# Optimization experiments

Hardware: AMD Instinct MI355X
Metric: run time of the kernel (lower is better)

Reference implementation:

```python
import jax, jax.numpy as jnp
import numpy as np

# Dimensions (match input_specs / init_kwargs)
B, T, M, H, E, K = 4, 2048, 1024, 2048, 8, 2
CAP_FACTOR = 1.0  # tutel default capacity_factor
S = B * T
C = int(K * CAP_FACTOR * ((S + E - 1) // E))  # per-expert capacity (tutel Top-k gate)


def setup_inputs() -> dict:
    key = jax.random.key(0)
    ks = jax.random.split(key, 4)
    x = jax.random.normal(ks[0], (B, T, M), jnp.float32)
    wg = jax.random.normal(ks[1], (M, E), jnp.float32) / np.sqrt(M)
    w1 = jax.random.normal(ks[2], (E, M, H), jnp.float32) / np.sqrt(M)
    b1 = jnp.zeros((E, H), jnp.float32)
    w2 = jax.random.normal(ks[3], (E, H, M), jnp.float32) / np.sqrt(H)
    b2 = jnp.zeros((E, M), jnp.float32)
    return {"x": x, "wg": wg, "w1": w1, "b1": b1, "w2": w2, "b2": b2}


def reference(x, wg, w1, b1, w2, b2):
    xf = x.reshape(S, M)
    # ---- Top-k gate (fp32 gate) ----
    logits = xf.astype(jnp.float32) @ wg                 # [S, E]
    scores = jax.nn.softmax(logits, axis=-1)
    topv, topi = jax.lax.top_k(scores, K)                # [S, K]
    gates = topv / (jnp.sum(topv, axis=-1, keepdims=True) + 1e-9)  # normalized top-k gates

    # ---- Dispatch into [E, C, M] buffer with capacity-based token dropping ----
    buf = jnp.zeros((E, C, M), xf.dtype)
    offset = jnp.zeros((E,), jnp.int32)  # tokens already placed per expert (previous slots)
    pos_list, keep_list = [], []
    for j in range(K):  # small fixed loop over top-k slots
        e = topi[:, j]                                   # [S]
        m = jax.nn.one_hot(e, E, dtype=jnp.int32)        # [S, E]
        pos = jnp.sum(jnp.cumsum(m, axis=0) * m, axis=1) - 1 + offset[e]  # position within expert
        offset = offset + jnp.sum(m, axis=0)
        keep = pos < C                                   # drop tokens over capacity
        posc = jnp.minimum(pos, C - 1)
        buf = buf.at[e, posc].add(xf * keep[:, None].astype(xf.dtype))
        pos_list.append(posc)
        keep_list.append(keep)

    # ---- Grouped expert FFN: relu(x W1 + b1) W2 + b2 ----
    h = jax.nn.relu(jnp.einsum('ecm,emh->ech', buf, w1) + b1[:, None, :])  # [E, C, H]
    y = jnp.einsum('ech,ehm->ecm', h, w2) + b2[:, None, :]                 # [E, C, M]

    # ---- Combine with gate weights ----
    out = jnp.zeros_like(xf)
    for j in range(K):
        g = gates[:, j] * keep_list[j].astype(xf.dtype)
        out = out + g[:, None] * y[topi[:, j], pos_list[j]]

    out = out.reshape(B, T, M)
    # result = log_softmax(sum over model_dim, over token dim)
    return jax.nn.log_softmax(jnp.sum(out, axis=2), axis=1)   # [B, T]
```

## Files before the change

kernel.cpp:

```cpp
#include <hip/hip_runtime.h>
#include <hip/hip_bf16.h>
#include <cstdint>
#include <cstddef>

constexpr int Bb = 4;
constexpr int Tt = 2048;
constexpr int Mm = 1024;
constexpr int Hh = 2048;
constexpr int Ee = 8;
constexpr int Ss = Bb * Tt;
constexpr int Cc = 2048;

typedef __attribute__((ext_vector_type(4))) float f32x4;
typedef __attribute__((ext_vector_type(8))) short bf16x8;

__device__ inline void load_lds16(const void* g, void* l) {
    __builtin_amdgcn_global_load_lds(
        (const __attribute__((address_space(1))) unsigned int*)g,
        (__attribute__((address_space(3))) unsigned int*)l, 16, 0, 0);
}

__global__ __launch_bounds__(256) void k_w1t(const float* __restrict__ w1,
                                             __hip_bfloat16* __restrict__ w1t) {
    __shared__ float tile[64][65];
    int e = blockIdx.z, m0 = blockIdx.y * 64, h0 = blockIdx.x * 64;
    int t = threadIdx.x;
    const float* src = w1 + (size_t)e * Mm * Hh;
    #pragma unroll
    for (int i = 0; i < 4; i++) {
        int idx = t + i * 256;
        int r = idx >> 4, c4 = idx & 15;
        float4 v = *(const float4*)(src + (size_t)(m0 + r) * Hh + h0 + c4 * 4);
        tile[r][c4 * 4 + 0] = v.x; tile[r][c4 * 4 + 1] = v.y;
        tile[r][c4 * 4 + 2] = v.z; tile[r][c4 * 4 + 3] = v.w;
    }
    __syncthreads();
    __hip_bfloat16* dst = w1t + (size_t)e * Hh * Mm;
    #pragma unroll
    for (int i = 0; i < 2; i++) {
        int idx = t + i * 256;
        int r = idx >> 3, c8 = idx & 7;
        __hip_bfloat16 tmp[8];
        #pragma unroll
        for (int k = 0; k < 8; k++) tmp[k] = __float2bfloat16(tile[c8 * 8 + k][r]);
        uint4 vv; __builtin_memcpy(&vv, tmp, 16);
        *(uint4*)(dst + (size_t)(h0 + r) * Mm + m0 + c8 * 8) = vv;
    }
}

__global__ void k_w2sum(const float* __restrict__ w2, float* __restrict__ w2sum) {
    int wave = threadIdx.x >> 6, lane = threadIdx.x & 63;
    int r = blockIdx.x * 4 + wave;
    const float4* p = (const float4*)(w2 + (size_t)r * Mm);
    float s = 0.f;
    #pragma unroll
    for (int i = 0; i < 4; i++) { float4 v = p[lane + i * 64]; s += v.x + v.y + v.z + v.w; }
    #pragma unroll
    for (int off = 32; off; off >>= 1) s += __shfl_down(s, off);
    if (lane == 0) w2sum[r] = s;
}

__global__ void k_b2sum(const float* __restrict__ b2, float* __restrict__ b2sum) {
    int e = blockIdx.x; int lane = threadIdx.x;
    const float4* p = (const float4*)(b2 + (size_t)e * Mm);
    float s = 0.f;
    #pragma unroll
    for (int i = 0; i < 4; i++) { float4 v = p[lane + i * 64]; s += v.x + v.y + v.z + v.w; }
    #pragma unroll
    for (int off = 32; off; off >>= 1) s += __shfl_down(s, off);
    if (lane == 0) b2sum[e] = s;
}

__global__ __launch_bounds__(256) void k_gate(const float* __restrict__ x,
                                              const float* __restrict__ wg,
                                              int* __restrict__ esel, float* __restrict__ gates) {
    int s = (blockIdx.x * 256 + threadIdx.x) >> 6;
    int lane = threadIdx.x & 63;
    const float4* xr = (const float4*)(x + (size_t)s * Mm);
    const float4* wgr = (const float4*)wg;
    float acc[8];
    #pragma unroll
    for (int e = 0; e < 8; e++) acc[e] = 0.f;
    #pragma unroll
    for (int i = 0; i < 4; i++) {
        float4 xv = xr[lane + i * 64];
        int mbase = (lane + i * 64) * 4;
        #pragma unroll
        for (int k = 0; k < 4; k++) {
            int m = mbase + k;
            float xm = (k == 0) ? xv.x : (k == 1) ? xv.y : (k == 2) ? xv.z : xv.w;
            float4 w0 = wgr[m * 2], w1v = wgr[m * 2 + 1];
            acc[0] += xm * w0.x;  acc[1] += xm * w0.y;  acc[2] += xm * w0.z;  acc[3] += xm * w0.w;
            acc[4] += xm * w1v.x; acc[5] += xm * w1v.y; acc[6] += xm * w1v.z; acc[7] += xm * w1v.w;
        }
    }
    #pragma unroll
    for (int off = 32; off; off >>= 1)
        #pragma unroll
        for (int e = 0; e < 8; e++) acc[e] += __shfl_down(acc[e], off);
    if (lane == 0) {
        float mx = acc[0];
        #pragma unroll
        for (int e = 1; e < 8; e++) mx = fmaxf(mx, acc[e]);
        float p[8], se = 0.f;
        #pragma unroll
        for (int e = 0; e < 8; e++) { p[e] = expf(acc[e] - mx); se += p[e]; }
        float inv = 1.f / se;
        #pragma unroll
        for (int e = 0; e < 8; e++) p[e] *= inv;
        int i0 = 0; float v0 = p[0];
        #pragma unroll
        for (int e = 1; e < 8; e++) if (p[e] > v0) { v0 = p[e]; i0 = e; }
        int i1 = -1; float v1 = -1.f;
        #pragma unroll
        for (int e = 0; e < 8; e++) if (e != i0 && p[e] > v1) { v1 = p[e]; i1 = e; }
        float den = v0 + v1 + 1e-9f;
        esel[s] = i0; esel[Ss + s] = i1;
        gates[s] = v0 / den; gates[Ss + s] = v1 / den;
    }
}

__global__ __launch_bounds__(256) void k_posA(const int* __restrict__ esel,
                                              int* __restrict__ lrank, int* __restrict__ blockhist) {
    int b = blockIdx.x, t = threadIdx.x;
    int d = b * 256 + t;
    int e = esel[d];
    int wave = t >> 6, lane = t & 63;
    __shared__ int wh[4][8];
    unsigned long long mymask = 0;
    #pragma unroll
    for (int q = 0; q < 8; q++) {
        unsigned long long m = __ballot(e == q);
        if (q == e) mymask = m;
        if (lane == 0) wh[wave][q] = (int)__popcll(m);
    }
    __syncthreads();
    int prefix = (int)__popcll(mymask & ((1ull << lane) - 1ull));
    for (int w = 0; w < wave; w++) prefix += wh[w][e];
    lrank[d] = prefix;
    if (t < 8) blockhist[b * 8 + t] = wh[0][t] + wh[1][t] + wh[2][t] + wh[3][t];
}

__global__ void k_posB(const int* __restrict__ blockhist, int* __restrict__ blockbase) {
    int q = threadIdx.x;
    if (q < 8) {
        int run = 0;
        for (int b = 0; b < 64; b++) {
            blockbase[b * 8 + q] = run;
            run += blockhist[b * 8 + q];
        }
    }
}

__global__ __launch_bounds__(128) void k_scatter(const float* __restrict__ x,
                                                 const int* __restrict__ esel,
                                                 const int* __restrict__ lrank,
                                                 const int* __restrict__ blockbase,
                                                 int* __restrict__ pos,
                                                 __hip_bfloat16* __restrict__ xbuf) {
    int d = blockIdx.x;
    __shared__ int sp, se;
    if (threadIdx.x == 0) {
        int e = esel[d];
        int p = blockbase[(d >> 8) * 8 + e] + lrank[d];
        pos[d] = p; sp = p; se = e;
    }
    __syncthreads();
    int p = sp;
    if (p >= Cc) return;
    int e = se;
    int s = d & (Ss - 1);
    int t = threadIdx.x;
    const float4* xr = (const float4*)(x + (size_t)s * Mm);
    float4 a = xr[t * 2], b = xr[t * 2 + 1];
    __hip_bfloat16 tmp[8];
    tmp[0] = __float2bfloat16(a.x); tmp[1] = __float2bfloat16(a.y);
    tmp[2] = __float2bfloat16(a.z); tmp[3] = __float2bfloat16(a.w);
    tmp[4] = __float2bfloat16(b.x); tmp[5] = __float2bfloat16(b.y);
    tmp[6] = __float2bfloat16(b.z); tmp[7] = __float2bfloat16(b.w);
    uint4 v;
    __builtin_memcpy(&v, tmp, 16);
    *(uint4*)(xbuf + ((size_t)e * Cc + p) * Mm + t * 8) = v;
}

__global__ __launch_bounds__(256) void k_gemm(
    const __hip_bfloat16* __restrict__ xbuf, const __hip_bfloat16* __restrict__ w1t,
    const float* __restrict__ b1, const float* __restrict__ w2sum,
    float* __restrict__ rowsum) {
    __shared__ __align__(16) __hip_bfloat16 As[128 * 32];
    __shared__ __align__(16) __hip_bfloat16 Bs[128 * 32];
    int e = blockIdx.y;
    int bid = blockIdx.x;
    int sq = bid >> 4, in16 = bid & 15;
    int hb = (sq & 3) * 4 + (in16 & 3);
    int cb = (sq >> 2) * 4 + (in16 >> 2);
    int c0 = cb * 128, h0 = hb * 128;
    int t = threadIdx.x;
    int wave = t >> 6, lane = t & 63;
    int wm = wave >> 1, wn = wave & 1;
    int r16 = lane & 15, quad = lane >> 4;
    const __hip_bfloat16* Ab = xbuf + (size_t)e * Cc * Mm;
    const __hip_bfloat16* Bp = w1t + (size_t)e * Hh * Mm;
    f32x4 acc[4][4];
    #pragma unroll
    for (int i = 0; i < 4; i++)
        #pragma unroll
        for (int j = 0; j < 4; j++) acc[i][j] = (f32x4){0.f, 0.f, 0.f, 0.f};

    for (int k0 = 0; k0 < Mm; k0 += 32) {
        #pragma unroll
        for (int p = 0; p < 2; ++p) {
            int ci = t + p * 256;
            int row = ci >> 2, q = ci & 3;
            load_lds16(Ab + (size_t)(c0 + row) * Mm + k0 + q * 8, As + ci * 8);
            load_lds16(Bp + (size_t)(h0 + row) * Mm + k0 + q * 8, Bs + ci * 8);
        }
        __syncthreads();
        bf16x8 af[4], bfr[4];
        #pragma unroll
        for (int mi = 0; mi < 4; mi++)
            af[mi] = *(const bf16x8*)(As + (wm * 64 + mi * 16 + r16) * 32 + quad * 8);
        #pragma unroll
        for (int ni = 0; ni < 4; ni++)
            bfr[ni] = *(const bf16x8*)(Bs + (wn * 64 + ni * 16 + r16) * 32 + quad * 8);
        #pragma unroll
        for (int mi = 0; mi < 4; mi++)
            #pragma unroll
            for (int ni = 0; ni < 4; ni++)
                acc[mi][ni] = __builtin_amdgcn_mfma_f32_16x16x32_bf16(af[mi], bfr[ni], acc[mi][ni], 0, 0, 0);
        __syncthreads();
    }

    float b1v[4], wsv[4];
    #pragma unroll
    for (int ni = 0; ni < 4; ni++) {
        int hg = h0 + wn * 64 + ni * 16 + r16;
        b1v[ni] = b1[e * Hh + hg];
        wsv[ni] = w2sum[e * Hh + hg];
    }
    #pragma unroll
    for (int mi = 0; mi < 4; mi++) {
        #pragma unroll
        for (int r = 0; r < 4; r++) {
            float val = 0.f;
            #pragma unroll
            for (int ni = 0; ni < 4; ni++) {
                float sv = acc[mi][ni][r] + b1v[ni];
                val += fmaxf(sv, 0.f) * wsv[ni];
            }
            #pragma unroll
            for (int off = 1; off < 16; off <<= 1) val += __shfl_xor(val, off);
            if (r16 == 0) {
                int cg = c0 + wm * 64 + mi * 16 + quad * 4 + r;
                atomicAdd(&rowsum[e * Cc + cg], val);
            }
        }
    }
}

__global__ __launch_bounds__(1024) void k_final(
    const int* __restrict__ esel, const int* __restrict__ pos,
    const float* __restrict__ gates, const float* __restrict__ rowsum,
    const float* __restrict__ b2sum, float* __restrict__ out) {
    int b = blockIdx.x; int t = threadIdx.x;
    __shared__ float red[1024];
    float vv[2];
    #pragma unroll
    for (int i = 0; i < 2; i++) {
        int tok = t + i * 1024;
        int s = b * Tt + tok;
        float acc = 0.f;
        #pragma unroll
        for (int j = 0; j < 2; j++) {
            int d = j * Ss + s;
            int p = pos[d];
            if (p < Cc) {
                int e = esel[d];
                acc += gates[d] * (rowsum[e * Cc + p] + b2sum[e]);
            }
        }
        vv[i] = acc;
    }
    float m = fmaxf(vv[0], vv[1]);
    red[t] = m; __syncthreads();
    for (int st = 512; st; st >>= 1) { if (t < st) red[t] = fmaxf(red[t], red[t + st]); __syncthreads(); }
    float mx = red[0];
    __syncthreads();
    float se = expf(vv[0] - mx) + expf(vv[1] - mx);
    red[t] = se; __syncthreads();
    for (int st = 512; st; st >>= 1) { if (t < st) red[t] += red[t + st]; __syncthreads(); }
    float lse = logf(red[0]);
    #pragma unroll
    for (int i = 0; i < 2; i++) {
        int tok = t + i * 1024;
        out[b * Tt + tok] = vv[i] - mx - lse;
    }
}

extern "C" void kernel_launch(void* const* d_in, const int* in_sizes, int n_in,
                              void* d_out, int out_size, void* d_ws, size_t ws_size,
                              hipStream_t stream) {
    const float* x  = (const float*)d_in[0];
    const float* wg = (const float*)d_in[1];
    const float* w1 = (const float*)d_in[2];
    const float* b1 = (const float*)d_in[3];
    const float* w2 = (const float*)d_in[4];
    const float* b2 = (const float*)d_in[5];
    float* out = (float*)d_out;

    char* ws = (char*)d_ws;
    size_t off = 0;
    auto alloc = [&](size_t bytes) -> void* {
        void* p = ws + off;
        off += (bytes + 255) & ~(size_t)255;
        return p;
    };
    float* w2sum    = (float*)alloc((size_t)Ee * Hh * 4);
    float* b2sum    = (float*)alloc(Ee * 4);
    int*   esel     = (int*)alloc((size_t)2 * Ss * 4);
    int*   lrank    = (int*)alloc((size_t)2 * Ss * 4);
    int*   blockhist= (int*)alloc((size_t)64 * 8 * 4);
    int*   blockbase= (int*)alloc((size_t)64 * 8 * 4);
    int*   pos      = (int*)alloc((size_t)2 * Ss * 4);
    float* gates    = (float*)alloc((size_t)2 * Ss * 4);
    float* rowsum   = (float*)alloc((size_t)Ee * Cc * 4);
    __hip_bfloat16* w1t  = (__hip_bfloat16*)alloc((size_t)Ee * Hh * Mm * 2);
    __hip_bfloat16* xbuf = (__hip_bfloat16*)alloc((size_t)Ee * Cc * Mm * 2);

    hipMemsetAsync(rowsum, 0, (size_t)Ee * Cc * 4, stream);
    k_w1t<<<dim3(Hh / 64, Mm / 64, Ee), 256, 0, stream>>>(w1, w1t);
    k_w2sum<<<Ee * Hh / 4, 256, 0, stream>>>(w2, w2sum);
    k_b2sum<<<Ee, 64, 0, stream>>>(b2, b2sum);
    k_gate<<<Ss / 4, 256, 0, stream>>>(x, wg, esel, gates);
    k_posA<<<64, 256, 0, stream>>>(esel, lrank, blockhist);
    k_posB<<<1, 64, 0, stream>>>(blockhist, blockbase);
    k_scatter<<<2 * Ss, 128, 0, stream>>>(x, esel, lrank, blockbase, pos, xbuf);
    k_gemm<<<dim3(16 * 16, Ee), 256, 0, stream>>>(xbuf, w1t, b1, w2sum, rowsum);
    k_final<<<Bb, 1024, 0, stream>>>(esel, pos, gates, rowsum, b2sum, out);
}
```

Before: 323.8 us.

## Widen GEMM K-tile with XOR-swizzled LDS, fuse bf16 cast into gate, merge small kernels

```diff
diff --git a/kernel.cpp b/kernel.cpp
--- a/kernel.cpp
+++ b/kernel.cpp
@@ -48,32 +48,35 @@
     }
 }
 
-__global__ void k_w2sum(const float* __restrict__ w2, float* __restrict__ w2sum) {
+__global__ void k_w2sum(const float* __restrict__ w2, const float* __restrict__ b2,
+                        float* __restrict__ w2sum, float* __restrict__ b2sum) {
     int wave = threadIdx.x >> 6, lane = threadIdx.x & 63;
-    int r = blockIdx.x * 4 + wave;
-    const float4* p = (const float4*)(w2 + (size_t)r * Mm);
-    float s = 0.f;
-    #pragma unroll
-    for (int i = 0; i < 4; i++) { float4 v = p[lane + i * 64]; s += v.x + v.y + v.z + v.w; }
-    #pragma unroll
-    for (int off = 32; off; off >>= 1) s += __shfl_down(s, off);
-    if (lane == 0) w2sum[r] = s;
-}
-
-__global__ void k_b2sum(const float* __restrict__ b2, float* __restrict__ b2sum) {
-    int e = blockIdx.x; int lane = threadIdx.x;
-    const float4* p = (const float4*)(b2 + (size_t)e * Mm);
-    float s = 0.f;
-    #pragma unroll
-    for (int i = 0; i < 4; i++) { float4 v = p[lane + i * 64]; s += v.x + v.y + v.z + v.w; }
-    #pragma unroll
-    for (int off = 32; off; off >>= 1) s += __shfl_down(s, off);
-    if (lane == 0) b2sum[e] = s;
+    if (blockIdx.x < Ee * Hh / 4) {
+        int r = blockIdx.x * 4 + wave;
+        const float4* p = (const float4*)(w2 + (size_t)r * Mm);
+        float s = 0.f;
+        #pragma unroll
+        for (int i = 0; i < 4; i++) { float4 v = p[lane + i * 64]; s += v.x + v.y + v.z + v.w; }
+        #pragma unroll
+        for (int off = 32; off; off >>= 1) s += __shfl_down(s, off);
+        if (lane == 0) w2sum[r] = s;
+    } else {
+        int e = wave * 2 + (lane >> 5);
+        int l = lane & 31;
+        const float4* p = (const float4*)(b2 + (size_t)e * Mm);
+        float s = 0.f;
+        #pragma unroll
+        for (int i = 0; i < 8; i++) { float4 v = p[l + i * 32]; s += v.x + v.y + v.z + v.w; }
+        #pragma unroll
+        for (int off = 16; off; off >>= 1) s += __shfl_down(s, off);
+        if (l == 0) b2sum[e] = s;
+    }
 }
 
 __global__ __launch_bounds__(256) void k_gate(const float* __restrict__ x,
                                               const float* __restrict__ wg,
-                                              int* __restrict__ esel, float* __restrict__ gates) {
+                                              int* __restrict__ esel, float* __restrict__ gates,
+                                              __hip_bfloat16* __restrict__ xbf) {
     int s = (blockIdx.x * 256 + threadIdx.x) >> 6;
     int lane = threadIdx.x & 63;
     const float4* xr = (const float4*)(x + (size_t)s * Mm);
@@ -84,6 +87,11 @@
     #pragma unroll
     for (int i = 0; i < 4; i++) {
         float4 xv = xr[lane + i * 64];
+        __hip_bfloat16 tb[4];
+        tb[0] = __float2bfloat16(xv.x); tb[1] = __float2bfloat16(xv.y);
+        tb[2] = __float2bfloat16(xv.z); tb[3] = __float2bfloat16(xv.w);
+        uint2 u; __builtin_memcpy(&u, tb, 8);
+        *(uint2*)(xbf + (size_t)s * Mm + (lane + i * 64) * 4) = u;
         int mbase = (lane + i * 64) * 4;
         #pragma unroll
         for (int k = 0; k < 4; k++) {
@@ -152,43 +160,33 @@
     }
 }
 
-__global__ __launch_bounds__(128) void k_scatter(const float* __restrict__ x,
+__global__ __launch_bounds__(128) void k_scatter(const __hip_bfloat16* __restrict__ xbf,
                                                  const int* __restrict__ esel,
                                                  const int* __restrict__ lrank,
                                                  const int* __restrict__ blockbase,
                                                  int* __restrict__ pos,
                                                  __hip_bfloat16* __restrict__ xbuf) {
-    int d = blockIdx.x;
-    __shared__ int sp, se;
-    if (threadIdx.x == 0) {
+    int s = blockIdx.x;
+    __shared__ int sp[2], se[2];
+    if (threadIdx.x < 2) {
+        int d = threadIdx.x * Ss + s;
         int e = esel[d];
         int p = blockbase[(d >> 8) * 8 + e] + lrank[d];
-        pos[d] = p; sp = p; se = e;
+        pos[d] = p; sp[threadIdx.x] = p; se[threadIdx.x] = e;
     }
     __syncthreads();
-    int p = sp;
-    if (p >= Cc) return;
-    int e = se;
-    int s = d & (Ss - 1);
     int t = threadIdx.x;
-    const float4* xr = (const float4*)(x + (size_t)s * Mm);
-    float4 a = xr[t * 2], b = xr[t * 2 + 1];
-    __hip_bfloat16 tmp[8];
-    tmp[0] = __float2bfloat16(a.x); tmp[1] = __float2bfloat16(a.y);
-    tmp[2] = __float2bfloat16(a.z); tmp[3] = __float2bfloat16(a.w);
-    tmp[4] = __float2bfloat16(b.x); tmp[5] = __float2bfloat16(b.y);
-    tmp[6] = __float2bfloat16(b.z); tmp[7] = __float2bfloat16(b.w);
-    uint4 v;
-    __builtin_memcpy(&v, tmp, 16);
-    *(uint4*)(xbuf + ((size_t)e * Cc + p) * Mm + t * 8) = v;
+    uint4 v = *(const uint4*)(xbf + (size_t)s * Mm + t * 8);
+    if (sp[0] < Cc) *(uint4*)(xbuf + ((size_t)se[0] * Cc + sp[0]) * Mm + t * 8) = v;
+    if (sp[1] < Cc) *(uint4*)(xbuf + ((size_t)se[1] * Cc + sp[1]) * Mm + t * 8) = v;
 }
 
 __global__ __launch_bounds__(256) void k_gemm(
     const __hip_bfloat16* __restrict__ xbuf, const __hip_bfloat16* __restrict__ w1t,
     const float* __restrict__ b1, const float* __restrict__ w2sum,
     float* __restrict__ rowsum) {
-    __shared__ __align__(16) __hip_bfloat16 As[128 * 32];
-    __shared__ __align__(16) __hip_bfloat16 Bs[128 * 32];
+    __shared__ __align__(16) __hip_bfloat16 As[128 * 64];
+    __shared__ __align__(16) __hip_bfloat16 Bs[128 * 64];
     int e = blockIdx.y;
     int bid = blockIdx.x;
     int sq = bid >> 4, in16 = bid & 15;
@@ -207,27 +205,37 @@
         #pragma unroll
         for (int j = 0; j < 4; j++) acc[i][j] = (f32x4){0.f, 0.f, 0.f, 0.f};
 
-    for (int k0 = 0; k0 < Mm; k0 += 32) {
-        #pragma unroll
-        for (int p = 0; p < 2; ++p) {
-            int ci = t + p * 256;
-            int row = ci >> 2, q = ci & 3;
+    for (int k0 = 0; k0 < Mm; k0 += 64) {
+        #pragma unroll
+        for (int p = 0; p < 4; ++p) {
+            int ci = p * 256 + t;
+            int row = ci >> 3, qs = ci & 7;
+            int q = qs ^ (row & 7);
             load_lds16(Ab + (size_t)(c0 + row) * Mm + k0 + q * 8, As + ci * 8);
             load_lds16(Bp + (size_t)(h0 + row) * Mm + k0 + q * 8, Bs + ci * 8);
         }
         __syncthreads();
-        bf16x8 af[4], bfr[4];
-        #pragma unroll
-        for (int mi = 0; mi < 4; mi++)
-            af[mi] = *(const bf16x8*)(As + (wm * 64 + mi * 16 + r16) * 32 + quad * 8);
-        #pragma unroll
-        for (int ni = 0; ni < 4; ni++)
-            bfr[ni] = *(const bf16x8*)(Bs + (wn * 64 + ni * 16 + r16) * 32 + quad * 8);
-        #pragma unroll
-        for (int mi = 0; mi < 4; mi++)
-            #pragma unroll
-            for (int ni = 0; ni < 4; ni++)
-                acc[mi][ni] = __builtin_amdgcn_mfma_f32_16x16x32_bf16(af[mi], bfr[ni], acc[mi][ni], 0, 0, 0);
+        #pragma unroll
+        for (int kk = 0; kk < 2; kk++) {
+            bf16x8 af[4], bfr[4];
+            #pragma unroll
+            for (int mi = 0; mi < 4; mi++) {
+                int row = wm * 64 + mi * 16 + r16;
+                int qx = (kk * 4 + quad) ^ (row & 7);
+                af[mi] = *(const bf16x8*)(As + row * 64 + qx * 8);
+            }
+            #pragma unroll
+            for (int ni = 0; ni < 4; ni++) {
+                int row = wn * 64 + ni * 16 + r16;
+                int qx = (kk * 4 + quad) ^ (row & 7);
+                bfr[ni] = *(const bf16x8*)(Bs + row * 64 + qx * 8);
+            }
+            #pragma unroll
+            for (int mi = 0; mi < 4; mi++)
+                #pragma unroll
+                for (int ni = 0; ni < 4; ni++)
+                    acc[mi][ni] = __builtin_amdgcn_mfma_f32_16x16x32_bf16(af[mi], bfr[ni], acc[mi][ni], 0, 0, 0);
+        }
         __syncthreads();
     }
 
@@ -324,17 +332,17 @@
     int*   pos      = (int*)alloc((size_t)2 * Ss * 4);
     float* gates    = (float*)alloc((size_t)2 * Ss * 4);
     float* rowsum   = (float*)alloc((size_t)Ee * Cc * 4);
+    __hip_bfloat16* xbf  = (__hip_bfloat16*)alloc((size_t)Ss * Mm * 2);
     __hip_bfloat16* w1t  = (__hip_bfloat16*)alloc((size_t)Ee * Hh * Mm * 2);
     __hip_bfloat16* xbuf = (__hip_bfloat16*)alloc((size_t)Ee * Cc * Mm * 2);
 
     hipMemsetAsync(rowsum, 0, (size_t)Ee * Cc * 4, stream);
     k_w1t<<<dim3(Hh / 64, Mm / 64, Ee), 256, 0, stream>>>(w1, w1t);
-    k_w2sum<<<Ee * Hh / 4, 256, 0, stream>>>(w2, w2sum);
-    k_b2sum<<<Ee, 64, 0, stream>>>(b2, b2sum);
-    k_gate<<<Ss / 4, 256, 0, stream>>>(x, wg, esel, gates);
+    k_w2sum<<<Ee * Hh / 4 + 1, 256, 0, stream>>>(w2, b2, w2sum, b2sum);
+    k_gate<<<Ss / 4, 256, 0, stream>>>(x, wg, esel, gates, xbf);
     k_posA<<<64, 256, 0, stream>>>(esel, lrank, blockhist);
     k_posB<<<1, 64, 0, stream>>>(blockhist, blockbase);
-    k_scatter<<<2 * Ss, 128, 0, stream>>>(x, esel, lrank, blockbase, pos, xbuf);
+    k_scatter<<<Ss, 128, 0, stream>>>(xbf, esel, lrank, blockbase, pos, xbuf);
     k_gemm<<<dim3(16 * 16, Ee), 256, 0, stream>>>(xbuf, w1t, b1, w2sum, rowsum);
     k_final<<<Bb, 1024, 0, stream>>>(esel, pos, gates, rowsum, b2sum, out);
 }
```

Result: slower. 332.2 us (+2.6%).
